# Kernel tuning notes

Measured on AMD Instinct MI355X. Metric: run time of the kernel, lower is better.

The kernel has to match this reference:

```python
import jax, jax.numpy as jnp
import numpy as np

SOFTCAP = 50.0  # GEMMA2_TANH_SCALE
N_HEADS = 16

def _rope(x, cos, sin):
    # x: [B,S,H,D]; cos/sin: [S,D/2]; interleaved complex pairs as in apply_rotary_emb
    x0 = x[..., 0::2]
    x1 = x[..., 1::2]
    c = cos[None, :, None, :]
    s = sin[None, :, None, :]
    r0 = x0 * c - x1 * s
    r1 = x0 * s + x1 * c
    return jnp.stack([r0, r1], axis=-1).reshape(x.shape)

def setup_inputs() -> dict:
    key = jax.random.key(0)
    ks = jax.random.split(key, 5)
    B, S, DM = 1, 2048, 2048
    hd = DM // N_HEADS
    scale = 1.0 / np.sqrt(DM)
    x = jax.random.normal(ks[0], (B, S, DM), jnp.float32)
    wq = jax.random.normal(ks[1], (DM, DM), jnp.float32) * scale
    wk = jax.random.normal(ks[2], (DM, DM), jnp.float32) * scale
    wv = jax.random.normal(ks[3], (DM, DM), jnp.float32) * scale
    wo = jax.random.normal(ks[4], (DM, DM), jnp.float32) * scale
    # rotary tables, theta=10000 as in llama
    inv_freq = 10000.0 ** (-jnp.arange(0, hd, 2, dtype=jnp.float32) / hd)
    ang = jnp.arange(S, dtype=jnp.float32)[:, None] * inv_freq[None, :]
    return {"x": x, "wq": wq, "wk": wk, "wv": wv, "wo": wo,
            "freqs_cos": jnp.cos(ang), "freqs_sin": jnp.sin(ang)}

def reference(x, wq, wk, wv, wo, freqs_cos, freqs_sin):
    B, S, DM = x.shape
    H = N_HEADS
    hd = DM // H
    q = (x @ wq).reshape(B, S, H, hd)
    k = (x @ wk).reshape(B, S, H, hd)
    v = (x @ wv).reshape(B, S, H, hd)
    q = _rope(q, freqs_cos, freqs_sin)
    k = _rope(k, freqs_cos, freqs_sin)
    # scores [B,H,S,S]
    scores = jnp.einsum('bqhd,bkhd->bhqk', q, k) / jnp.sqrt(jnp.float32(hd))
    scores = SOFTCAP * jnp.tanh(scores / SOFTCAP)  # gemma2 tanh soft-cap
    causal = jnp.tril(jnp.ones((S, S), dtype=bool))
    scores = jnp.where(causal[None, None], scores, -jnp.inf)
    p = jax.nn.softmax(scores, axis=-1)
    o = jnp.einsum('bhqk,bkhd->bqhd', p, v).reshape(B, S, DM)
    return o @ wo
```

## Files before the change

kernel.cpp:

```cpp
#include <hip/hip_runtime.h>
#include <hip/hip_bf16.h>

typedef __attribute__((ext_vector_type(8))) short short8;
typedef __attribute__((ext_vector_type(4))) short short4v;
typedef __attribute__((ext_vector_type(4))) float f32x4;
typedef __attribute__((ext_vector_type(4))) float float4v;

#define S_LEN 2048
#define DMODEL 2048
#define N_HEADS 16
#define HEAD_DIM 128
#define NKT 32

__device__ __forceinline__ float bf2f(__hip_bfloat16 b) { return __bfloat162float(b); }
__device__ __forceinline__ __hip_bfloat16 f2bf(float f) { return __float2bfloat16(f); }
__device__ __forceinline__ short bfs(float f) {
    union { __hip_bfloat16 b; short s; } x; x.b = __float2bfloat16(f); return x.s;
}
__device__ __forceinline__ float sbf(short s) {
    union { short s; __hip_bfloat16 b; } x; x.s = s; return __bfloat162float(x.b);
}

#if __has_builtin(__builtin_amdgcn_global_load_lds)
#define HAVE_ASYNC_LDS 1
#else
#define HAVE_ASYNC_LDS 0
#endif

__device__ __forceinline__ void stage16(const __hip_bfloat16* g, __hip_bfloat16* ldsbase, int lane) {
#if HAVE_ASYNC_LDS
    __builtin_amdgcn_global_load_lds(
        (const __attribute__((address_space(1))) unsigned int*)g,
        (__attribute__((address_space(3))) unsigned int*)ldsbase,
        16, 0, 0);
#else
    *(short8*)((char*)ldsbase + lane * 16) = *(const short8*)g;
#endif
}

__global__ __launch_bounds__(256) void prep(const float* __restrict__ x,
                                            const float* __restrict__ w0,
                                            const float* __restrict__ w1,
                                            const float* __restrict__ w2,
                                            const float* __restrict__ w3,
                                            __hip_bfloat16* __restrict__ xb,
                                            __hip_bfloat16* __restrict__ o0,
                                            __hip_bfloat16* __restrict__ o1,
                                            __hip_bfloat16* __restrict__ o2,
                                            __hip_bfloat16* __restrict__ o3) {
    const int z = blockIdx.z;
    const int tid = threadIdx.x;
    if (z == 4) {
        size_t base = (((size_t)blockIdx.y * 32 + blockIdx.x) * 256 + tid) * 16;
        for (int i = 0; i < 4; ++i) {
            float4v v = *(const float4v*)(x + base + i * 4);
            short4v p;
            p.x = bfs(v.x); p.y = bfs(v.y); p.z = bfs(v.z); p.w = bfs(v.w);
            *(short4v*)((short*)xb + base + i * 4) = p;
        }
        return;
    }
    const float* in = (z == 0) ? w0 : (z == 1) ? w1 : (z == 2) ? w2 : w3;
    __hip_bfloat16* out = (z == 0) ? o0 : (z == 1) ? o1 : (z == 2) ? o2 : o3;
    __shared__ short tile[64][68];
    const int bx = blockIdx.x * 64;
    const int by = blockIdx.y * 64;
    const int c4 = (tid & 15) * 4;
    for (int rr = 0; rr < 4; ++rr) {
        int r = (tid >> 4) + rr * 16;
        float4v v = *(const float4v*)(in + (size_t)(by + r) * DMODEL + bx + c4);
        short4v p;
        p.x = bfs(v.x); p.y = bfs(v.y); p.z = bfs(v.z); p.w = bfs(v.w);
        *(short4v*)&tile[r][c4] = p;
    }
    __syncthreads();
    const int oc = tid >> 2;
    const int s0 = (tid & 3) * 16;
    short8 a, b;
    for (int i = 0; i < 8; ++i) ((short*)&a)[i] = tile[s0 + i][oc];
    for (int i = 0; i < 8; ++i) ((short*)&b)[i] = tile[s0 + 8 + i][oc];
    *(short8*)((short*)out + (size_t)(bx + oc) * DMODEL + by + s0) = a;
    *(short8*)((short*)out + (size_t)(bx + oc) * DMODEL + by + s0 + 8) = b;
}


#define CFENCE asm volatile("" ::: "memory")
#define BARRIER do { CFENCE; __builtin_amdgcn_s_barrier(); CFENCE; } while (0)
#define WAIT_LGKM0 asm volatile("s_waitcnt lgkmcnt(0)" ::: "memory")
#define WAIT_VM(n) asm volatile("s_waitcnt vmcnt(" #n ")" ::: "memory")


#define STAGE_A8(buf, half, kt) do {                                                        \
    const __hip_bfloat16* gpA_ = A + (size_t)(m0 + (half) * 128 + wave * 16 + rsel) * DMODEL \
                                 + (kt) * 64 + gsrc;                                        \
    __hip_bfloat16* lpA_ = (__hip_bfloat16*)(smem + ((buf) * 2 + (half)) * 8192 + wave * 1024); \
    stage16(gpA_, lpA_, lane);                                                              \
    stage16(gpA_ + (size_t)8 * DMODEL, lpA_ + 512, lane);                                   \
} while (0)

#define STAGE_B8(buf, half, kt) do {                                                        \
    const __hip_bfloat16* gpB_ = Bt + (size_t)(n0 + (half) * 128 + wave * 16 + rsel) * DMODEL \
                                 + (kt) * 64 + gsrc;                                        \
    __hip_bfloat16* lpB_ = (__hip_bfloat16*)(smem + 32768 + ((buf) * 2 + (half)) * 8192 + wave * 1024); \
    stage16(gpB_, lpB_, lane);                                                              \
    stage16(gpB_ + (size_t)8 * DMODEL, lpB_ + 512, lane);                                   \
} while (0)

#define LDA_ALL(buf) do {                                                                   \
    const char* ab_ = (const char*)(smem + ((buf) * 2 + wr) * 8192);                        \
    _Pragma("unroll")                                                                       \
    for (int mt_ = 0; mt_ < 8; ++mt_) {                                                     \
        const int rowL_ = mt_ * 16 + lane15;                                                \
        const int r7_ = rowL_ & 7;                                                          \
        af[mt_][0] = *(const short8*)(ab_ + rowL_ * 128 + ((quad ^ r7_) * 16));             \
        af[mt_][1] = *(const short8*)(ab_ + rowL_ * 128 + (((4 + quad) ^ r7_) * 16));       \
    }                                                                                       \
} while (0)

#define LDB_ALL(buf) do {                                                                   \
    const char* bb_ = (const char*)(smem + 32768 + ((buf) * 2 + hb) * 8192);                \
    _Pragma("unroll")                                                                       \
    for (int nt_ = 0; nt_ < 4; ++nt_) {                                                     \
        const int rowL_ = wc1 * 64 + nt_ * 16 + lane15;                                     \
        const int r7_ = rowL_ & 7;                                                          \
        bfr[nt_][0] = *(const short8*)(bb_ + rowL_ * 128 + ((quad ^ r7_) * 16));            \
        bfr[nt_][1] = *(const short8*)(bb_ + rowL_ * 128 + (((4 + quad) ^ r7_) * 16));      \
    }                                                                                       \
} while (0)

#define MFMAQ(mb, nb) do {                                                                  \
    _Pragma("unroll")                                                                       \
    for (int mt_ = 0; mt_ < 4; ++mt_) {                                                     \
        _Pragma("unroll")                                                                   \
        for (int nt_ = 0; nt_ < 2; ++nt_) {                                                 \
            acc[(mb) + mt_][(nb) + nt_] = __builtin_amdgcn_mfma_f32_16x16x32_bf16(          \
                af[(mb) + mt_][0], bfr[(nb) + nt_][0], acc[(mb) + mt_][(nb) + nt_], 0, 0, 0); \
            acc[(mb) + mt_][(nb) + nt_] = __builtin_amdgcn_mfma_f32_16x16x32_bf16(          \
                af[(mb) + mt_][1], bfr[(nb) + nt_][1], acc[(mb) + mt_][(nb) + nt_], 0, 0, 0); \
        }                                                                                   \
    }                                                                                       \
} while (0)

#define GROUP(g, cur, nxt) do {                                                             \
    const int g_ = (g);                                                                     \
    const bool stB_ = (g_ + 1 < NKT);                                                       \
    const bool stA_ = (g_ + 2 < NKT);                                                       \
    LDA_ALL(cur);                                                                           \
    LDB_ALL(cur);                                                                           \
    if (stB_) { STAGE_B8(nxt, 0, g_ + 1); STAGE_B8(nxt, 1, g_ + 1); }                       \
    __builtin_amdgcn_s_setprio(1);                                                          \
    MFMAQ(0, 0); MFMAQ(4, 0);                                                               \
    __builtin_amdgcn_s_setprio(0);                                                          \
    WAIT_LGKM0;                             \
    BARRIER;                     \
    if (stA_) { STAGE_A8(cur, 0, g_ + 2); STAGE_A8(cur, 1, g_ + 2); }                       \
    __builtin_amdgcn_s_setprio(1);                                                          \
    MFMAQ(0, 2); MFMAQ(4, 2);                                                               \
    __builtin_amdgcn_s_setprio(0);                                                          \
    if (stA_) { WAIT_VM(4); }               \
    else if (stB_) { WAIT_VM(0); }          \
    BARRIER;                                                                                \
} while (0)

__global__ __launch_bounds__(512, 2) void gemm_qkv_8ph(const __hip_bfloat16* __restrict__ A,
                                                       const __hip_bfloat16* __restrict__ Bq,
                                                       const __hip_bfloat16* __restrict__ Bk,
                                                       const __hip_bfloat16* __restrict__ Bv,
                                                       __hip_bfloat16* __restrict__ Cq,
                                                       __hip_bfloat16* __restrict__ Ck,
                                                       __hip_bfloat16* __restrict__ Cvt,
                                                       const float* __restrict__ fc,
                                                       const float* __restrict__ fs) {
    __shared__ alignas(16) short smem[65536];

    const int tid = threadIdx.x;
    const int wave = tid >> 6;
    const int lane = tid & 63;
    const int lane15 = lane & 15;
    const int quad = lane >> 4;
    const int wr = wave >> 2;
    const int wc = wave & 3;
    const int wc1 = wc & 1;
    const int hb = wc >> 1;
    const int rsel = lane >> 3;
    const int gsrc = ((lane & 7) ^ rsel) * 8;

    const int which = blockIdx.x >> 3;
    const int n0 = (blockIdx.x & 7) * 256;
    const int m0 = blockIdx.y * 256;
    const __hip_bfloat16* Bt = (which == 0) ? Bq : (which == 1) ? Bk : Bv;

    short8 af[8][2];
    short8 bfr[4][2];
    f32x4 acc[8][4];

    STAGE_A8(0, 0, 0);
    STAGE_B8(0, 0, 0);
    STAGE_A8(0, 1, 0);
    STAGE_B8(0, 1, 0);
    STAGE_A8(1, 0, 1);
    STAGE_A8(1, 1, 1);
#pragma unroll
    for (int i = 0; i < 8; ++i)
#pragma unroll
        for (int j = 0; j < 4; ++j)
            acc[i][j] = {0.f, 0.f, 0.f, 0.f};
    WAIT_VM(4);
    BARRIER;

#pragma unroll 1
    for (int g = 0; g < NKT; g += 2) {
        GROUP(g, 0, 1);
        GROUP(g + 1, 1, 0);
    }

    if (which < 2) {
        __hip_bfloat16* C = (which == 0) ? Cq : Ck;
#pragma unroll
        for (int mt = 0; mt < 8; ++mt)
#pragma unroll
            for (int nt = 0; nt < 4; ++nt) {
                int col = n0 + wc * 64 + nt * 16 + lane15;
                int j = (col & 127) >> 1;
                bool odd = col & 1;
#pragma unroll
                for (int i = 0; i < 4; ++i) {
                    int row = m0 + wr * 128 + mt * 16 + quad * 4 + i;
                    float v = acc[mt][nt][i];
                    float p = __shfl_xor(v, 1, 64);
                    float c = fc[row * 64 + j];
                    float sn = fs[row * 64 + j];
                    float r = odd ? (p * sn + v * c) : (v * c - p * sn);
                    C[(size_t)row * DMODEL + col] = f2bf(r);
                }
            }
    } else {
#pragma unroll
        for (int mt = 0; mt < 8; ++mt) {
            int rowbase = m0 + wr * 128 + mt * 16 + quad * 4;
#pragma unroll
            for (int nt = 0; nt < 4; ++nt) {
                int col = n0 + wc * 64 + nt * 16 + lane15;
                short4v pk;
                pk.x = bfs(acc[mt][nt][0]);
                pk.y = bfs(acc[mt][nt][1]);
                pk.z = bfs(acc[mt][nt][2]);
                pk.w = bfs(acc[mt][nt][3]);
                *(short4v*)((short*)Cvt + (size_t)col * S_LEN + rowbase) = pk;
            }
        }
    }
}

__global__ __launch_bounds__(256) void gemm_out(const __hip_bfloat16* __restrict__ A,
                                                const __hip_bfloat16* __restrict__ Bt,
                                                float* __restrict__ C) {
    __shared__ alignas(16) __hip_bfloat16 As[2][128 * 32];
    __shared__ alignas(16) __hip_bfloat16 Bs[2][64 * 32];
    const int tid = threadIdx.x;
    const int wave = tid >> 6;
    const int lane = tid & 63;
    const int lane15 = lane & 15;
    const int quad = lane >> 4;
    const int m0 = blockIdx.y * 128;
    const int n0 = blockIdx.x * 64;
    const int wm = (wave >> 1) * 64;
    const int wn = (wave & 1) * 32;
    f32x4 acc[4][2];
    for (int i = 0; i < 4; ++i)
        for (int j = 0; j < 2; ++j)
            acc[i][j] = {0.f, 0.f, 0.f, 0.f};
    const int rA = lane >> 2;
    const int cA = (lane & 3) * 8;
    for (int k0 = 0; k0 < DMODEL; k0 += 64) {
        __syncthreads();
        for (int h = 0; h < 2; ++h) {
            int kk = k0 + h * 32;
            for (int c = 0; c < 3; ++c) {
                int chunk = wave * 3 + c;
                if (chunk < 8) {
                    int r = chunk * 16 + rA;
                    stage16(A + (size_t)(m0 + r) * DMODEL + kk + cA, As[h] + chunk * 512, lane);
                } else {
                    int r = (chunk - 8) * 16 + rA;
                    stage16(Bt + (size_t)(n0 + r) * DMODEL + kk + cA, Bs[h] + (chunk - 8) * 512, lane);
                }
            }
        }
#if HAVE_ASYNC_LDS
        asm volatile("s_waitcnt vmcnt(0)" ::: "memory");
#endif
        __syncthreads();
        for (int h = 0; h < 2; ++h) {
            short8 af[4], bfr[2];
            for (int mt = 0; mt < 4; ++mt)
                af[mt] = *(const short8*)(As[h] + (wm + mt * 16 + lane15) * 32 + quad * 8);
            for (int nt = 0; nt < 2; ++nt)
                bfr[nt] = *(const short8*)(Bs[h] + (wn + nt * 16 + lane15) * 32 + quad * 8);
            for (int mt = 0; mt < 4; ++mt)
                for (int nt = 0; nt < 2; ++nt)
                    acc[mt][nt] = __builtin_amdgcn_mfma_f32_16x16x32_bf16(af[mt], bfr[nt], acc[mt][nt], 0, 0, 0);
        }
    }
    for (int mt = 0; mt < 4; ++mt)
        for (int nt = 0; nt < 2; ++nt)
            for (int i = 0; i < 4; ++i) {
                int row = m0 + wm + mt * 16 + quad * 4 + i;
                int col = n0 + wn + nt * 16 + lane15;
                C[(size_t)row * DMODEL + col] = acc[mt][nt][i];
            }
}

__global__ __launch_bounds__(256) void flash_attn(const __hip_bfloat16* __restrict__ Q,
                                                  const __hip_bfloat16* __restrict__ Kb,
                                                  const __hip_bfloat16* __restrict__ Vt,
                                                  __hip_bfloat16* __restrict__ O) {
    __shared__ alignas(16) short Ks[32][136];
    __shared__ alignas(16) short Vs[128][40];
    __shared__ alignas(16) short Pl[4][16][40];
    const int tid = threadIdx.x;
    const int wave = tid >> 6;
    const int lane = tid & 63;
    const int lane15 = lane & 15;
    const int quad = lane >> 4;
    const int bx = blockIdx.x;
    const int u = bx & 255;
    const int head = u & 15;
    const int qp = u >> 4;
    const int qb = (bx < 256) ? (31 - qp) : qp;
    const int qbase = qb * 64;
    const int q0w = qbase + wave * 16;
    const int nkt = 2 * qb + 2;
    const float K1 = 0.08838834764831845f * (1.0f / 25.0f);

    const __hip_bfloat16* Qh = Q + (size_t)q0w * DMODEL + head * HEAD_DIM;
    short8 qf[4];
    for (int kk = 0; kk < 4; ++kk)
        qf[kk] = *(const short8*)(Qh + (size_t)lane15 * DMODEL + kk * 32 + quad * 8);

    f32x4 acc[8];
    for (int i = 0; i < 8; ++i) acc[i] = {0.f, 0.f, 0.f, 0.f};
    float lpart[4] = {0.f, 0.f, 0.f, 0.f};

    const int krow = tid >> 3, kcol = (tid & 7) * 16;
    const int vrow = tid >> 1, vcol = (tid & 1) * 16;
    const __hip_bfloat16* Kg = Kb + (size_t)krow * DMODEL + head * HEAD_DIM + kcol;
    const __hip_bfloat16* Vg = Vt + (size_t)(head * HEAD_DIM + vrow) * S_LEN + vcol;

    short8 gk0 = *(const short8*)(Kg);
    short8 gk1 = *(const short8*)(Kg + 8);
    short8 gv0 = *(const short8*)(Vg);
    short8 gv1 = *(const short8*)(Vg + 8);

    for (int kt = 0; kt < nkt; ++kt) {
        const int kb = kt * 32;
        __syncthreads();
        *(short8*)&Ks[krow][kcol] = gk0;
        *(short8*)&Ks[krow][kcol + 8] = gk1;
        *(short8*)&Vs[vrow][vcol] = gv0;
        *(short8*)&Vs[vrow][vcol + 8] = gv1;
        __syncthreads();

        if (kt + 1 < nkt) {
            const __hip_bfloat16* Kg2 = Kg + (size_t)(kb + 32) * DMODEL;
            const __hip_bfloat16* Vg2 = Vg + kb + 32;
            gk0 = *(const short8*)(Kg2);
            gk1 = *(const short8*)(Kg2 + 8);
            gv0 = *(const short8*)(Vg2);
            gv1 = *(const short8*)(Vg2 + 8);
        }

        if (kb <= q0w + 15) {
            f32x4 sc[2];
            sc[0] = {0.f, 0.f, 0.f, 0.f};
            sc[1] = {0.f, 0.f, 0.f, 0.f};
            for (int c = 0; c < 2; ++c)
                for (int kk = 0; kk < 4; ++kk) {
                    short8 kf = *(const short8*)&Ks[c * 16 + lane15][kk * 32 + quad * 8];
                    sc[c] = __builtin_amdgcn_mfma_f32_16x16x32_bf16(qf[kk], kf, sc[c], 0, 0, 0);
                }

            const bool masked = (kb + 31 > q0w);
            const int key0 = kb + lane15;
            const int key1 = kb + 16 + lane15;
            for (int i = 0; i < 4; ++i) {
                float e0 = __expf(sc[0][i] * K1);
                float e1 = __expf(sc[1][i] * K1);
                float c0 = __builtin_fmaf(-100.0f, __builtin_amdgcn_rcpf(e0 + 1.0f), 40.0f);
                float c1 = __builtin_fmaf(-100.0f, __builtin_amdgcn_rcpf(e1 + 1.0f), 40.0f);
                float p0 = __expf(c0);
                float p1 = __expf(c1);
                if (masked) {
                    int q = q0w + quad * 4 + i;
                    if (key0 > q) p0 = 0.f;
                    if (key1 > q) p1 = 0.f;
                }
                short b0 = bfs(p0), b1 = bfs(p1);
                lpart[i] += sbf(b0) + sbf(b1);
                Pl[wave][quad * 4 + i][lane15] = b0;
                Pl[wave][quad * 4 + i][16 + lane15] = b1;
            }
            asm volatile("s_waitcnt lgkmcnt(0)" ::: "memory");
            short8 pf = *(const short8*)&Pl[wave][lane15][quad * 8];
            asm volatile("" ::: "memory");
            for (int nt = 0; nt < 8; ++nt) {
                short8 vf = *(const short8*)&Vs[nt * 16 + lane15][quad * 8];
                acc[nt] = __builtin_amdgcn_mfma_f32_16x16x32_bf16(pf, vf, acc[nt], 0, 0, 0);
            }
        }
    }

    for (int i = 0; i < 4; ++i) {
        float l = lpart[i];
        l += __shfl_xor(l, 1, 64);
        l += __shfl_xor(l, 2, 64);
        l += __shfl_xor(l, 4, 64);
        l += __shfl_xor(l, 8, 64);
        float inv = 1.0f / l;
        int row = q0w + quad * 4 + i;
        for (int nt = 0; nt < 8; ++nt) {
            int col = head * HEAD_DIM + nt * 16 + lane15;
            O[(size_t)row * DMODEL + col] = f2bf(acc[nt][i] * inv);
        }
    }
}

extern "C" void kernel_launch(void* const* d_in, const int* in_sizes, int n_in,
                              void* d_out, int out_size, void* d_ws, size_t ws_size,
                              hipStream_t stream) {
    const float* x  = (const float*)d_in[0];
    const float* wq = (const float*)d_in[1];
    const float* wk = (const float*)d_in[2];
    const float* wv = (const float*)d_in[3];
    const float* wo = (const float*)d_in[4];
    const float* fc = (const float*)d_in[5];
    const float* fs = (const float*)d_in[6];
    float* out = (float*)d_out;

    char* ws = (char*)d_ws;
    const size_t MB8 = (size_t)2048 * 2048 * sizeof(__hip_bfloat16);
    __hip_bfloat16* wq_t = (__hip_bfloat16*)(ws + 0 * MB8);
    __hip_bfloat16* wk_t = (__hip_bfloat16*)(ws + 1 * MB8);
    __hip_bfloat16* wv_t = (__hip_bfloat16*)(ws + 2 * MB8);
    __hip_bfloat16* wo_t = (__hip_bfloat16*)(ws + 3 * MB8);
    __hip_bfloat16* s4   = (__hip_bfloat16*)(ws + 4 * MB8);
    __hip_bfloat16* s5   = (__hip_bfloat16*)(ws + 5 * MB8);
    __hip_bfloat16* s6   = (__hip_bfloat16*)(ws + 6 * MB8);
    __hip_bfloat16* x_bf = (__hip_bfloat16*)d_out;

    prep<<<dim3(32, 32, 5), 256, 0, stream>>>(x, wq, wk, wv, wo, x_bf, wq_t, wk_t, wv_t, wo_t);

    gemm_qkv_8ph<<<dim3(24, 8), 512, 0, stream>>>(x_bf, wq_t, wk_t, wv_t, s4, s5, s6, fc, fs);

    flash_attn<<<512, 256, 0, stream>>>(s4, s5, s6, wq_t);
    gemm_out<<<dim3(32, 16), 256, 0, stream>>>(wq_t, wo_t, out);
}
```

Baseline: 292.5 us.

## Split flash attention over two key ranges and merge partials in a combine kernel

Each attention block's key range is split into two chunks, which doubles the grid to 1024 blocks. Each chunk writes unnormalized fp32 accumulators and row sums to workspace, and a new combine kernel adds the partials, normalizes and writes bf16 for the output GEMM. The aim is more parallelism and better latency hiding on a GPU that was only lightly occupied. The cost is extra fp32 global traffic (two 16MB partial buffers written then read) and one more kernel launch. Correctness relies on the partials sharing a fixed softmax offset, since the combine does no max rescaling.

```diff
diff --git a/kernel.cpp b/kernel.cpp
--- a/kernel.cpp
+++ b/kernel.cpp
@@ -89,7 +89,6 @@
 #define WAIT_LGKM0 asm volatile("s_waitcnt lgkmcnt(0)" ::: "memory")
 #define WAIT_VM(n) asm volatile("s_waitcnt vmcnt(" #n ")" ::: "memory")
 
-
 #define STAGE_A8(buf, half, kt) do {                                                        \
     const __hip_bfloat16* gpA_ = A + (size_t)(m0 + (half) * 128 + wave * 16 + rsel) * DMODEL \
                                  + (kt) * 64 + gsrc;                                        \
@@ -151,14 +150,14 @@
     __builtin_amdgcn_s_setprio(1);                                                          \
     MFMAQ(0, 0); MFMAQ(4, 0);                                                               \
     __builtin_amdgcn_s_setprio(0);                                                          \
-    WAIT_LGKM0;                             \
-    BARRIER;                     \
+    WAIT_LGKM0;                                                                             \
+    BARRIER;                                                                                \
     if (stA_) { STAGE_A8(cur, 0, g_ + 2); STAGE_A8(cur, 1, g_ + 2); }                       \
     __builtin_amdgcn_s_setprio(1);                                                          \
     MFMAQ(0, 2); MFMAQ(4, 2);                                                               \
     __builtin_amdgcn_s_setprio(0);                                                          \
-    if (stA_) { WAIT_VM(4); }               \
-    else if (stB_) { WAIT_VM(0); }          \
+    if (stA_) { WAIT_VM(4); }                                                               \
+    else if (stB_) { WAIT_VM(0); }                                                          \
     BARRIER;                                                                                \
 } while (0)
 
@@ -314,7 +313,10 @@
 __global__ __launch_bounds__(256) void flash_attn(const __hip_bfloat16* __restrict__ Q,
                                                   const __hip_bfloat16* __restrict__ Kb,
                                                   const __hip_bfloat16* __restrict__ Vt,
-                                                  __hip_bfloat16* __restrict__ O) {
+                                                  float* __restrict__ N0,
+                                                  float* __restrict__ N1,
+                                                  float* __restrict__ L0,
+                                                  float* __restrict__ L1) {
     __shared__ alignas(16) short Ks[32][136];
     __shared__ alignas(16) short Vs[128][40];
     __shared__ alignas(16) short Pl[4][16][40];
@@ -324,14 +326,19 @@
     const int lane15 = lane & 15;
     const int quad = lane >> 4;
     const int bx = blockIdx.x;
-    const int u = bx & 255;
+    const int chunk = bx >> 9;
+    const int bxl = bx & 511;
+    const int u = bxl & 255;
     const int head = u & 15;
     const int qp = u >> 4;
-    const int qb = (bx < 256) ? (31 - qp) : qp;
-    const int qbase = qb * 64;
-    const int q0w = qbase + wave * 16;
-    const int nkt = 2 * qb + 2;
+    const int qb = (bxl < 256) ? (31 - qp) : qp;
+    const int q0w = qb * 64 + wave * 16;
+    const int k_lo = chunk ? (qb + 1) : 0;
+    const int k_hi = chunk ? (2 * qb + 2) : (qb + 1);
     const float K1 = 0.08838834764831845f * (1.0f / 25.0f);
+
+    float* __restrict__ Nw = chunk ? N1 : N0;
+    float* __restrict__ Lw = chunk ? L1 : L0;
 
     const __hip_bfloat16* Qh = Q + (size_t)q0w * DMODEL + head * HEAD_DIM;
     short8 qf[4];
@@ -347,12 +354,13 @@
     const __hip_bfloat16* Kg = Kb + (size_t)krow * DMODEL + head * HEAD_DIM + kcol;
     const __hip_bfloat16* Vg = Vt + (size_t)(head * HEAD_DIM + vrow) * S_LEN + vcol;
 
-    short8 gk0 = *(const short8*)(Kg);
-    short8 gk1 = *(const short8*)(Kg + 8);
-    short8 gv0 = *(const short8*)(Vg);
-    short8 gv1 = *(const short8*)(Vg + 8);
-
-    for (int kt = 0; kt < nkt; ++kt) {
+    const int kb0 = k_lo * 32;
+    short8 gk0 = *(const short8*)(Kg + (size_t)kb0 * DMODEL);
+    short8 gk1 = *(const short8*)(Kg + (size_t)kb0 * DMODEL + 8);
+    short8 gv0 = *(const short8*)(Vg + kb0);
+    short8 gv1 = *(const short8*)(Vg + kb0 + 8);
+
+    for (int kt = k_lo; kt < k_hi; ++kt) {
         const int kb = kt * 32;
         __syncthreads();
         *(short8*)&Ks[krow][kcol] = gk0;
@@ -361,7 +369,7 @@
         *(short8*)&Vs[vrow][vcol + 8] = gv1;
         __syncthreads();
 
-        if (kt + 1 < nkt) {
+        if (kt + 1 < k_hi) {
             const __hip_bfloat16* Kg2 = Kg + (size_t)(kb + 32) * DMODEL;
             const __hip_bfloat16* Vg2 = Vg + kb + 32;
             gk0 = *(const short8*)(Kg2);
@@ -416,13 +424,39 @@
         l += __shfl_xor(l, 2, 64);
         l += __shfl_xor(l, 4, 64);
         l += __shfl_xor(l, 8, 64);
-        float inv = 1.0f / l;
         int row = q0w + quad * 4 + i;
+        if (lane15 == 0) Lw[(head << 11) + row] = l;
         for (int nt = 0; nt < 8; ++nt) {
             int col = head * HEAD_DIM + nt * 16 + lane15;
-            O[(size_t)row * DMODEL + col] = f2bf(acc[nt][i] * inv);
-        }
-    }
+            Nw[(size_t)row * DMODEL + col] = acc[nt][i];
+        }
+    }
+}
+
+__global__ __launch_bounds__(256) void attn_combine(const float* __restrict__ N0,
+                                                    const float* __restrict__ N1,
+                                                    const float* __restrict__ L0,
+                                                    const float* __restrict__ L1,
+                                                    __hip_bfloat16* __restrict__ Aout) {
+    size_t i0 = ((size_t)blockIdx.x * 256 + threadIdx.x) * 8;
+    const int row = (int)(i0 >> 11);
+    const int head = (int)((i0 >> 7) & 15);
+    const float l = L0[(head << 11) + row] + L1[(head << 11) + row];
+    const float inv = 1.0f / l;
+    float4v a0 = *(const float4v*)(N0 + i0);
+    float4v a1 = *(const float4v*)(N1 + i0);
+    float4v b0 = *(const float4v*)(N0 + i0 + 4);
+    float4v b1 = *(const float4v*)(N1 + i0 + 4);
+    short8 o;
+    ((short*)&o)[0] = bfs((a0.x + a1.x) * inv);
+    ((short*)&o)[1] = bfs((a0.y + a1.y) * inv);
+    ((short*)&o)[2] = bfs((a0.z + a1.z) * inv);
+    ((short*)&o)[3] = bfs((a0.w + a1.w) * inv);
+    ((short*)&o)[4] = bfs((b0.x + b1.x) * inv);
+    ((short*)&o)[5] = bfs((b0.y + b1.y) * inv);
+    ((short*)&o)[6] = bfs((b0.z + b1.z) * inv);
+    ((short*)&o)[7] = bfs((b0.w + b1.w) * inv);
+    *(short8*)((short*)Aout + i0) = o;
 }
 
 extern "C" void kernel_launch(void* const* d_in, const int* in_sizes, int n_in,
@@ -446,12 +480,18 @@
     __hip_bfloat16* s4   = (__hip_bfloat16*)(ws + 4 * MB8);
     __hip_bfloat16* s5   = (__hip_bfloat16*)(ws + 5 * MB8);
     __hip_bfloat16* s6   = (__hip_bfloat16*)(ws + 6 * MB8);
+    float* N1 = (float*)(ws + 7 * MB8);
+    float* L0 = (float*)(ws + 9 * MB8);
+    float* L1 = L0 + 2048 * 16;
     __hip_bfloat16* x_bf = (__hip_bfloat16*)d_out;
+    float* N0 = (float*)d_out;
 
     prep<<<dim3(32, 32, 5), 256, 0, stream>>>(x, wq, wk, wv, wo, x_bf, wq_t, wk_t, wv_t, wo_t);
 
     gemm_qkv_8ph<<<dim3(24, 8), 512, 0, stream>>>(x_bf, wq_t, wk_t, wv_t, s4, s5, s6, fc, fs);
 
-    flash_attn<<<512, 256, 0, stream>>>(s4, s5, s6, wq_t);
-    gemm_out<<<dim3(32, 16), 256, 0, stream>>>(wq_t, wo_t, out);
-}
+    flash_attn<<<1024, 256, 0, stream>>>(s4, s5, s6, N0, N1, L0, L1);
+
+    attn_combine<<<2048, 256, 0, stream>>>(N0, N1, L0, L1, s4);
+    gemm_out<<<dim3(32, 16), 256, 0, stream>>>(s4, wo_t, out);
+}
```

Result: faster. 277.7 us (-5.1%).
